# Kernel optimization log

Measured on AMD Instinct MI355X. Metric: run time of the kernel, lower is better.

## Reference

```python
import jax, jax.numpy as jnp
import numpy as np


def _dht(x):
    # Hartley transform via full fftn over ALL dims (matches torch dht2d(x, dim=None))
    f = jnp.fft.fftn(x)
    return f.real + f.imag


def setup_inputs() -> dict:
    key = jax.random.key(0)
    ks = jax.random.split(key, 5)
    B, H, W, C = 2, 128, 256, 768
    nb, fac = 8, 1
    bs = C // nb
    scale = 0.02
    x = jax.random.normal(ks[0], (B, H, W, C), dtype=jnp.float32)
    w1 = scale * jax.random.normal(ks[1], (2, nb, bs, bs * fac), dtype=jnp.float32)
    b1 = scale * jax.random.normal(ks[2], (2, nb, bs * fac), dtype=jnp.float32)
    w2 = scale * jax.random.normal(ks[3], (2, nb, bs * fac, bs), dtype=jnp.float32)
    b2 = scale * jax.random.normal(ks[4], (2, nb, bs), dtype=jnp.float32)
    return {"x": x, "w1": w1, "b1": b1, "w2": w2, "b2": b2}


def reference(x, w1, b1, w2, b2):
    SPARSITY = 0.01
    FRAC = 1.0  # hard_thresholding_fraction
    bias = x
    B, H, W, C = x.shape
    nb = w1.shape[1]
    bs = C // nb
    xf = x.astype(jnp.float32)

    X_k = _dht(xf).reshape(B, H, W, nb, bs)
    X_nk = jnp.roll(jnp.flip(xf, axis=(1, 2)), shift=(1, 1), axis=(1, 2)).reshape(B, H, W, nb, bs)

    total = H // 2 + 1
    kept = int(total * FRAC)
    r0, r1 = total - kept, min(total + kept, H)  # row slice clamps like torch slicing

    a = X_k[:, r0:r1, :kept]    # [B, Hs, kept, nb, bs]
    an = X_nk[:, r0:r1, :kept]

    ein = lambda t, w: jnp.einsum('bhwni,nio->bhwno', t, w)

    o1_k = jax.nn.relu(0.5 * (ein(a, w1[0]) - ein(an, w1[1]) + ein(a, w1[1]) + ein(an, w1[0])) + b1[0])
    o1_nk = jax.nn.relu(0.5 * (ein(an, w1[0]) - ein(a, w1[1]) + ein(an, w1[1]) + ein(a, w1[0])) + b1[1])

    o2_k = 0.5 * (ein(o1_k, w2[0]) - ein(o1_nk, w2[1]) + ein(o1_k, w2[1]) + ein(o1_nk, w2[0])) + b2[0]
    # NOTE: source genuinely uses o2_k (not o1_k) in two terms here; kept faithful.
    o2_nk = 0.5 * (ein(o1_nk, w2[0]) - ein(o2_k, w2[1]) + ein(o1_nk, w2[1]) + ein(o2_k, w2[0])) + b2[1]

    s = o2_k + o2_nk
    # softshrink
    s = jnp.sign(s) * jnp.maximum(jnp.abs(s) - SPARSITY, 0.0)

    full = jnp.zeros((B, H, W, nb, bs), jnp.float32).at[:, r0:r1, :kept].set(s)
    full = full.reshape(B, H, W, C)
    out = _dht(full) / full.size  # idht2d with dim=None: normalize by numel
    return out.astype(x.dtype) + bias
```

## Files before the change

kernel.cpp:

```cpp
#include <hip/hip_runtime.h>

#define BB 2
#define HH 128
#define WW 256
#define CC 768
#define NB 8
#define BS 96
#define WKEPT 65
#define NPTS (BB*HH*WKEPT)
#define NTOT ((size_t)BB*HH*WW*CC)
#define TWOPI 6.283185307179586f

#define P1_TW (9*127*8)
#define P7_TW (16*65*8)

__device__ __forceinline__ unsigned short f2bf(float f) {
    unsigned int u = __float_as_uint(f);
    u += 0x7fffu + ((u >> 16) & 1u);
    return (unsigned short)(u >> 16);
}
__device__ __forceinline__ float bf2f(unsigned short s) {
    return __uint_as_float((unsigned int)s << 16);
}

__global__ __launch_bounds__(256) void k_weights(
    const float* __restrict__ w2, const float* __restrict__ b2,
    float* __restrict__ WKP, float* __restrict__ WKM, float* __restrict__ BEFF)
{
    const int n = blockIdx.x;
    const int tid = threadIdx.x;
    __shared__ float m_s[BS*BS];

    const float* w2a = w2 + (size_t)(0*NB + n)*BS*BS;
    const float* w2b = w2 + (size_t)(1*NB + n)*BS*BS;
    for (int idx = tid; idx < BS*BS; idx += 256)
        m_s[idx] = 0.5f*(w2a[idx] - w2b[idx]);
    __syncthreads();

    for (int idx = tid; idx < BS*BS; idx += 256) {
        int i = idx / BS, o = idx - i*BS;
        float p_io = 0.5f*(w2a[idx] + w2b[idx]);
        float m_io = m_s[idx];
        float accK = 0.f, accN = 0.f;
        for (int j = 0; j < BS; ++j) {
            float p_ij = 0.5f*(w2a[i*BS + j] + w2b[i*BS + j]);
            float mjo  = m_s[j*BS + o];
            accK += p_ij * mjo;
            accN += m_s[i*BS + j] * mjo;
        }
        float valK = p_io + accK;
        float valN = p_io + m_io + accN;
        WKP[n*BS*BS + idx] = 0.5f*(valK + valN);
        WKM[n*BS*BS + idx] = 0.5f*(valK - valN);
    }
    if (tid < BS) {
        const float* b2a = b2 + (0*NB + n)*BS;
        const float* b2b = b2 + (1*NB + n)*BS;
        float acc = b2a[tid] + b2b[tid];
        for (int j = 0; j < BS; ++j) acc += b2a[j] * m_s[j*BS + tid];
        BEFF[n*BS + tid] = acc;
    }
}

__global__ __launch_bounds__(256) void k_tw(
    float* __restrict__ c7t, float* __restrict__ s7t)
{
    int idx = blockIdx.x*256 + threadIdx.x;
    if (idx < P7_TW) {
        int j = idx & 7; int rest = idx >> 3;
        int wq = rest % 65; int wg = rest / 65;
        int ai = ((wg*8 + j) * wq) & 255;
        float sn, cs; sincosf(TWOPI * (float)ai / 256.0f, &sn, &cs);
        c7t[idx] = cs; s7t[idx] = sn;
    }
}

__global__ __launch_bounds__(256) void k_p1(
    const float* __restrict__ x, float2* __restrict__ out)
{
    const int tid = threadIdx.x;
    const int row = blockIdx.y;
    const int c0 = blockIdx.x * 16;
    __shared__ float2 tw[256];
    __shared__ float2 bufA[8*256];
    __shared__ float2 bufB[8*256];

    {
        float sn, cs; sincosf(TWOPI*(float)tid/256.f, &sn, &cs);
        tw[tid] = make_float2(cs, -sn);
    }
    const float* xr = x + (size_t)row * WW * CC + c0;
    for (int idx = tid; idx < 2048; idx += 256) {
        int l = idx & 7, w = idx >> 3;
        const float2 v = *(const float2*)(xr + (size_t)w*CC + 2*l);
        bufA[l*256 + w] = v;
    }
    __syncthreads();

    float2* src = bufA;
    float2* dst = bufB;
    const int t  = tid & 127;
    const int l0 = tid >> 7;
    #pragma unroll
    for (int st = 0; st < 8; ++st) {
        const int s = 1 << st;
        const int q = t & (s - 1);
        const int p = t >> st;
        const float2 w = tw[p << st];
        #pragma unroll
        for (int k = 0; k < 4; ++k) {
            int base = (l0 + 2*k) * 256;
            float2 a = src[base + q + s*p];
            float2 b = src[base + q + s*p + 128];
            float dx = a.x - b.x, dy = a.y - b.y;
            dst[base + q + 2*s*p]     = make_float2(a.x + b.x, a.y + b.y);
            dst[base + q + 2*s*p + s] = make_float2(dx*w.x - dy*w.y, dx*w.y + dy*w.x);
        }
        __syncthreads();
        float2* tmp = src; src = dst; dst = tmp;
    }
    for (int idx = tid; idx < 8*WKEPT; idx += 256) {
        int l = idx & 7, wp = idx >> 3;
        float2 Z  = src[l*256 + wp];
        float2 Zm = src[l*256 + ((256 - wp) & 255)];
        float2 U = make_float2(0.5f*(Z.x + Zm.x), 0.5f*(Z.y - Zm.y));
        float2 V = make_float2(0.5f*(Z.y + Zm.y), 0.5f*(Zm.x - Z.x));
        size_t g = (size_t)(row*WKEPT + wp)*CC + c0 + 2*l;
        out[g]     = U;
        out[g + 1] = V;
    }
}

#define LPB 4
__global__ __launch_bounds__(256) void k_cfft(
    const float2* __restrict__ in, float2* __restrict__ out)
{
    __shared__ float2 tw[CC];
    __shared__ float2 bufA[LPB*CC];
    __shared__ float2 bufB[LPB*CC];
    const int tid = threadIdx.x;
    const size_t line0 = (size_t)blockIdx.x * LPB;

    for (int t = tid; t < CC; t += 256) {
        float sn, cs; sincosf(TWOPI * (float)t / 768.0f, &sn, &cs);
        tw[t] = make_float2(cs, -sn);
    }
    for (int idx = tid; idx < LPB*CC; idx += 256) {
        int l = idx / CC, c = idx - l*CC;
        int m = c / 3, j = c - 3*m;
        bufA[l*CC + j*256 + m] = in[(line0 + l)*CC + c];
    }
    __syncthreads();

    float2* src = bufA;
    float2* dst = bufB;
    #pragma unroll
    for (int st = 0; st < 8; ++st) {
        const int s = 1 << st;
        const int h = 128 >> st;
        for (int item = tid; item < LPB*3*128; item += 256) {
            int sub = item >> 7;
            int t   = item & 127;
            int q = t & (s - 1);
            int p = t >> st;
            float2 a = src[sub*256 + q + s*p];
            float2 b = src[sub*256 + q + s*(p + h)];
            float2 w = tw[p * (3 << st)];
            float dx = a.x - b.x, dy = a.y - b.y;
            dst[sub*256 + q + s*(2*p)]     = make_float2(a.x + b.x, a.y + b.y);
            dst[sub*256 + q + s*(2*p + 1)] = make_float2(dx*w.x - dy*w.y, dx*w.y + dy*w.x);
        }
        __syncthreads();
        float2* tmp = src; src = dst; dst = tmp;
    }
    for (int idx = tid; idx < LPB*CC; idx += 256) {
        int l = idx / CC, cp = idx - l*CC;
        int r = cp & 255;
        float2 S0 = src[(l*3 + 0)*256 + r];
        float2 S1 = src[(l*3 + 1)*256 + r];
        float2 S2 = src[(l*3 + 2)*256 + r];
        float2 w1 = tw[cp];
        int i2 = 2*cp; if (i2 >= CC) i2 -= CC;
        float2 w2 = tw[i2];
        float fr = S0.x + w1.x*S1.x - w1.y*S1.y + w2.x*S2.x - w2.y*S2.y;
        float fi = S0.y + w1.x*S1.y + w1.y*S1.x + w2.x*S2.y + w2.y*S2.x;
        out[(line0 + l)*CC + cp] = make_float2(fr, fi);
    }
}

__global__ __launch_bounds__(256) void k_hb_c2a(
    const float2* __restrict__ in, float* __restrict__ aout)
{
    const int tid = threadIdx.x;
    const int wp = blockIdx.y;
    const int c0 = blockIdx.x * 8;
    __shared__ float2 tw[128];
    __shared__ float2 bufA[16*128];
    __shared__ float2 bufB[16*128];

    if (tid < 128) {
        float sn, cs; sincosf(TWOPI*(float)tid/128.f, &sn, &cs);
        tw[tid] = make_float2(cs, -sn);
    }
    for (int idx = tid; idx < 1024; idx += 256) {
        int cl = idx & 7, h = idx >> 3;
        float2 z0 = in[(size_t)((0*HH + h)*WKEPT + wp)*CC + c0 + cl];
        float2 z1 = in[(size_t)((1*HH + h)*WKEPT + wp)*CC + c0 + cl];
        bufA[(2*cl+0)*128 + h] = make_float2(z0.x+z1.x, z0.y+z1.y);
        bufA[(2*cl+1)*128 + h] = make_float2(z0.x-z1.x, z0.y-z1.y);
    }
    __syncthreads();

    float2* src = bufA;
    float2* dst = bufB;
    const int t  = tid & 63;
    const int l0 = tid >> 6;
    #pragma unroll
    for (int st = 0; st < 7; ++st) {
        const int s = 1 << st;
        const int q = t & (s - 1);
        const int p = t >> st;
        const float2 w = tw[p << st];
        #pragma unroll
        for (int k = 0; k < 4; ++k) {
            int base = (l0 + 4*k) * 128;
            float2 a = src[base + q + s*p];
            float2 b = src[base + q + s*p + 64];
            float dx = a.x - b.x, dy = a.y - b.y;
            dst[base + q + 2*s*p]     = make_float2(a.x + b.x, a.y + b.y);
            dst[base + q + 2*s*p + s] = make_float2(dx*w.x - dy*w.y, dx*w.y + dy*w.x);
        }
        __syncthreads();
        float2* tmp = src; src = dst; dst = tmp;
    }
    for (int idx = tid; idx < 2048; idx += 256) {
        int cl = idx & 7;
        int hp = (idx >> 3) & 127;
        int uv = idx >> 10;
        float2 z = src[(2*cl + uv)*128 + hp];
        aout[(size_t)((uv*HH + hp)*WKEPT + wp)*CC + c0 + cl] = z.x + z.y;
    }
}

__global__ __launch_bounds__(256) void k_hb_s2c(
    const float* __restrict__ sreal, float2* __restrict__ out)
{
    const int tid = threadIdx.x;
    const int wp = blockIdx.y;
    const int c0 = blockIdx.x * 16;
    __shared__ float2 tw[128];
    __shared__ float2 bufA[16*128];
    __shared__ float2 bufB[16*128];

    if (tid < 128) {
        float sn, cs; sincosf(TWOPI*(float)tid/128.f, &sn, &cs);
        tw[tid] = make_float2(cs, -sn);
    }
    for (int idx = tid; idx < 2048; idx += 256) {
        int cl = idx & 15, h = idx >> 4;
        float s0 = sreal[(size_t)((0*HH + h)*WKEPT + wp)*CC + c0 + cl];
        float s1 = sreal[(size_t)((1*HH + h)*WKEPT + wp)*CC + c0 + cl];
        bufA[cl*128 + h] = make_float2(s0 + s1, s0 - s1);
    }
    __syncthreads();

    float2* src = bufA;
    float2* dst = bufB;
    const int t  = tid & 63;
    const int l0 = tid >> 6;
    #pragma unroll
    for (int st = 0; st < 7; ++st) {
        const int s = 1 << st;
        const int q = t & (s - 1);
        const int p = t >> st;
        const float2 w = tw[p << st];
        #pragma unroll
        for (int k = 0; k < 4; ++k) {
            int base = (l0 + 4*k) * 128;
            float2 a = src[base + q + s*p];
            float2 b = src[base + q + s*p + 64];
            float dx = a.x - b.x, dy = a.y - b.y;
            dst[base + q + 2*s*p]     = make_float2(a.x + b.x, a.y + b.y);
            dst[base + q + 2*s*p + s] = make_float2(dx*w.x - dy*w.y, dx*w.y + dy*w.x);
        }
        __syncthreads();
        float2* tmp = src; src = dst; dst = tmp;
    }
    for (int idx = tid; idx < 2048; idx += 256) {
        int cl = idx & 15;
        int hp = idx >> 4;
        float2 A  = src[cl*128 + hp];
        float2 Zm = src[cl*128 + ((128 - hp) & 127)];
        float2 U = make_float2(0.5f*(A.x + Zm.x), 0.5f*(A.y - Zm.y));
        float2 V = make_float2(0.5f*(A.y + Zm.y), 0.5f*(Zm.x - A.x));
        out[(size_t)((0*HH + hp)*WKEPT + wp)*CC + c0 + cl] = U;
        out[(size_t)((1*HH + hp)*WKEPT + wp)*CC + c0 + cl] = V;
    }
}

__global__ __launch_bounds__(256, 6) void k_mlp(
    const float* __restrict__ a, const float* __restrict__ x,
    const float* __restrict__ w1, const float* __restrict__ b1,
    const float* __restrict__ WKP, const float* __restrict__ WKM,
    const float* __restrict__ BEFF, float* __restrict__ sout)
{
    const int tid = threadIdx.x;
    const int n = blockIdx.y;
    const int P0 = blockIdx.x * 64;
    __shared__ unsigned short SH[2*96*67];
    unsigned short* As = SH;
    unsigned short* Bs = SH + 96*67;

    for (int idx = tid; idx < 64*96; idx += 256) {
        int p = idx / 96, i = idx - p*96;
        int P = P0 + p;
        float av = a[(size_t)P*CC + n*BS + i];
        int b = P / (HH*WKEPT);
        int rem = P - b*(HH*WKEPT);
        int h = rem / WKEPT;
        int wq = rem - h*WKEPT;
        int hh2 = (HH - h) & (HH-1);
        int ww2 = (WW - wq) & (WW-1);
        float anv = x[(size_t)((b*HH + hh2)*WW + ww2)*CC + n*BS + i];
        As[i*67 + p] = f2bf(0.5f*(av + anv));
        Bs[i*67 + p] = f2bf(0.5f*(av - anv));
    }
    __syncthreads();

    const int lane = tid & 63;
    const int wv = __builtin_amdgcn_readfirstlane(tid >> 6);
    const int ob = wv * 24;

    float t1[24], t2[24];
    #pragma unroll
    for (int j = 0; j < 24; ++j) { t1[j] = 0.f; t2[j] = 0.f; }
    {
        const float* w10 = w1 + (size_t)(0*NB + n)*BS*BS + ob;
        const float* w11 = w1 + (size_t)(1*NB + n)*BS*BS + ob;
        #pragma unroll 2
        for (int i = 0; i < 96; ++i) {
            float Uv = bf2f(As[i*67 + lane]);
            float Vv = bf2f(Bs[i*67 + lane]);
            const float* r0 = w10 + i*BS;
            const float* r1 = w11 + i*BS;
            #pragma unroll
            for (int j = 0; j < 24; ++j) {
                t1[j] = fmaf(Uv, r0[j], t1[j]);
                t2[j] = fmaf(Vv, r1[j], t2[j]);
            }
        }
    }

    {
        const float* b1k = b1 + (0*NB + n)*BS + ob;
        const float* b1n = b1 + (1*NB + n)*BS + ob;
        float p2v[24], m2v[24];
        #pragma unroll
        for (int j = 0; j < 24; ++j) {
            float ok = fmaxf(t1[j] + t2[j] + b1k[j], 0.f);
            float on = fmaxf(t1[j] - t2[j] + b1n[j], 0.f);
            p2v[j] = ok + on;
            m2v[j] = ok - on;
        }
        __syncthreads();
        #pragma unroll
        for (int j = 0; j < 24; ++j) {
            As[(ob + j)*67 + lane] = f2bf(p2v[j]);
            Bs[(ob + j)*67 + lane] = f2bf(m2v[j]);
        }
        __syncthreads();
    }

    float acc[24];
    #pragma unroll
    for (int j = 0; j < 24; ++j) acc[j] = 0.f;
    {
        const float* wkp = WKP + n*BS*BS + ob;
        const float* wkm = WKM + n*BS*BS + ob;
        #pragma unroll 2
        for (int i = 0; i < 96; ++i) {
            float pv = bf2f(As[i*67 + lane]);
            float mv = bf2f(Bs[i*67 + lane]);
            const float* rk = wkp + i*BS;
            const float* rm = wkm + i*BS;
            #pragma unroll
            for (int j = 0; j < 24; ++j) {
                acc[j] = fmaf(pv, rk[j], fmaf(mv, rm[j], acc[j]));
            }
        }
    }

    {
        const float* be = BEFF + n*BS + ob;
        float r[24];
        #pragma unroll
        for (int j = 0; j < 24; ++j) {
            float v = acc[j] + be[j];
            float av2 = fabsf(v) - 0.01f;
            r[j] = (av2 > 0.f) ? copysignf(av2, v) : 0.f;
        }
        __syncthreads();
        float* Fs = (float*)SH;
        #pragma unroll
        for (int j = 0; j < 24; ++j)
            Fs[lane*97 + ob + j] = r[j];
        __syncthreads();
        for (int idx = tid; idx < 64*96; idx += 256) {
            int p2i = idx / 96, o = idx - p2i*96;
            sout[(size_t)(P0 + p2i)*CC + n*BS + o] = Fs[p2i*97 + o];
        }
    }
}

__global__ __launch_bounds__(256) void k_p7(
    const float2* __restrict__ A, const float* __restrict__ x,
    const float* __restrict__ c7t, const float* __restrict__ s7t,
    float* __restrict__ out)
{
    const int tid = threadIdx.x;
    const int ct = blockIdx.x % 3;
    const int wg = blockIdx.x / 3;
    const int rg = blockIdx.y;
    const int c  = ct*256 + tid;
    const int wpb = wg*8;
    const int row0 = rg*4;

    float accA[4][8], accB[4][8], acc128[4];
    #pragma unroll
    for (int r = 0; r < 4; ++r) {
        acc128[r] = 0.f;
        #pragma unroll
        for (int j = 0; j < 8; ++j) { accA[r][j] = 0.f; accB[r][j] = 0.f; }
    }

    const float2* A0 = A + (size_t)row0 * WKEPT * CC + c;
    const float4* cT = (const float4*)(c7t + (size_t)wg*65*8);
    const float4* sT = (const float4*)(s7t + (size_t)wg*65*8);
    for (int wq = 0; wq < 65; ++wq) {
        float4 c0 = cT[2*wq], c1 = cT[2*wq+1];
        float4 s0 = sT[2*wq], s1 = sT[2*wq+1];
        float sg = (wq & 1) ? -1.f : 1.f;
        #pragma unroll
        for (int r = 0; r < 4; ++r) {
            float2 v = A0[(size_t)(r*WKEPT + wq) * CC];
            float P = v.x + v.y;
            float M = v.y - v.x;
            float N = v.x - v.y;
            acc128[r] = fmaf(sg, P, acc128[r]);
            accA[r][0] = fmaf(P, c0.x, fmaf(M, s0.x, accA[r][0]));
            accB[r][0] = fmaf(P, c0.x, fmaf(N, s0.x, accB[r][0]));
            accA[r][1] = fmaf(P, c0.y, fmaf(M, s0.y, accA[r][1]));
            accB[r][1] = fmaf(P, c0.y, fmaf(N, s0.y, accB[r][1]));
            accA[r][2] = fmaf(P, c0.z, fmaf(M, s0.z, accA[r][2]));
            accB[r][2] = fmaf(P, c0.z, fmaf(N, s0.z, accB[r][2]));
            accA[r][3] = fmaf(P, c0.w, fmaf(M, s0.w, accA[r][3]));
            accB[r][3] = fmaf(P, c0.w, fmaf(N, s0.w, accB[r][3]));
            accA[r][4] = fmaf(P, c1.x, fmaf(M, s1.x, accA[r][4]));
            accB[r][4] = fmaf(P, c1.x, fmaf(N, s1.x, accB[r][4]));
            accA[r][5] = fmaf(P, c1.y, fmaf(M, s1.y, accA[r][5]));
            accB[r][5] = fmaf(P, c1.y, fmaf(N, s1.y, accB[r][5]));
            accA[r][6] = fmaf(P, c1.z, fmaf(M, s1.z, accA[r][6]));
            accB[r][6] = fmaf(P, c1.z, fmaf(N, s1.z, accB[r][6]));
            accA[r][7] = fmaf(P, c1.w, fmaf(M, s1.w, accA[r][7]));
            accB[r][7] = fmaf(P, c1.w, fmaf(N, s1.w, accB[r][7]));
        }
    }

    const float scale = 1.0f / 50331648.0f;
    #pragma unroll
    for (int r = 0; r < 4; ++r) {
        size_t base = (size_t)(row0 + r) * WW * CC + c;
        #pragma unroll
        for (int j = 0; j < 8; ++j) {
            int w = wpb + j;
            size_t g = base + (size_t)w*CC;
            out[g] = fmaf(accA[r][j], scale, x[g]);
            if (w != 0) {
                size_t g2 = base + (size_t)(256 - w)*CC;
                out[g2] = fmaf(accB[r][j], scale, x[g2]);
            }
        }
        if (wg == 0) {
            size_t g = base + (size_t)128*CC;
            out[g] = fmaf(acc128[r], scale, x[g]);
        }
    }
}

__global__ __launch_bounds__(256) void k_p7_fb(
    const float2* __restrict__ A, const float* __restrict__ x,
    float* __restrict__ out)
{
    const int tid = threadIdx.x;
    const int ct = blockIdx.x % 3;
    const int wg = blockIdx.x / 3;
    const int h = blockIdx.y, b = blockIdx.z;
    const int c = ct*256 + tid;
    __shared__ float cm[WKEPT][8];
    __shared__ float cp[WKEPT][8];
    for (int idx = tid; idx < WKEPT*8; idx += 256) {
        int wq = idx >> 3, j = idx & 7;
        int w = wg*8 + j;
        int ai = (w * wq) & 255;
        float sn, cse; sincosf(TWOPI * (float)ai / 256.f, &sn, &cse);
        cm[wq][j] = cse - sn;
        cp[wq][j] = cse + sn;
    }
    __syncthreads();
    float acc[8] = {0,0,0,0,0,0,0,0};
    const float2* Ab = A + (size_t)((b*HH + h)*WKEPT)*CC + c;
    for (int wq = 0; wq < WKEPT; ++wq) {
        float2 v = Ab[(size_t)wq*CC];
        const float4* m4 = (const float4*)(&cm[wq][0]);
        const float4* p4 = (const float4*)(&cp[wq][0]);
        #pragma unroll
        for (int jj = 0; jj < 2; ++jj) {
            float4 qm = m4[jj], qp = p4[jj];
            acc[4*jj+0] += v.x*qm.x + v.y*qp.x;
            acc[4*jj+1] += v.x*qm.y + v.y*qp.y;
            acc[4*jj+2] += v.x*qm.z + v.y*qp.z;
            acc[4*jj+3] += v.x*qm.w + v.y*qp.w;
        }
    }
    const float scale = 1.0f / 50331648.0f;
    size_t base = (size_t)(b*HH + h)*WW*CC + c;
    #pragma unroll
    for (int j = 0; j < 8; ++j) {
        int w = wg*8 + j;
        size_t g = base + (size_t)w*CC;
        out[g] = fmaf(acc[j], scale, x[g]);
    }
}

extern "C" void kernel_launch(void* const* d_in, const int* in_sizes, int n_in,
                              void* d_out, int out_size, void* d_ws, size_t ws_size,
                              hipStream_t stream)
{
    (void)in_sizes; (void)n_in; (void)out_size;
    const float* x  = (const float*)d_in[0];
    const float* w1 = (const float*)d_in[1];
    const float* b1 = (const float*)d_in[2];
    const float* w2 = (const float*)d_in[3];
    const float* b2 = (const float*)d_in[4];

    float*  ws     = (float*)d_ws;
    float2* Abuf   = (float2*)d_ws;
    float*  a_real = ws;
    float*  s_real = ws + (size_t)NPTS*CC;
    float*  W1P    = ws + 2*(size_t)NPTS*CC;
    float*  W1M    = W1P + NB*BS*BS;
    float*  WKP    = W1M + NB*BS*BS;
    float*  WKM    = WKP + NB*BS*BS;
    float*  BEFF   = WKM + NB*BS*BS;
    float*  c1t    = BEFF + NB*BS;
    float*  s1t    = c1t + P1_TW;
    float*  c7t    = s1t + P1_TW;
    float*  s7t    = c7t + P7_TW;

    const size_t need_bytes =
        ((size_t)2*NPTS*CC + 4*(size_t)NB*BS*BS + NB*BS + 2*P1_TW + 2*P7_TW)
        * sizeof(float);
    const bool fast = (ws_size >= need_bytes);

    float2* Bc   = (float2*)d_out;
    float*  outf = (float*)d_out;

    k_weights<<<dim3(NB), dim3(256), 0, stream>>>(w2, b2, WKP, WKM, BEFF);
    if (fast) {
        k_tw<<<dim3(33), dim3(256), 0, stream>>>(c7t, s7t);
    }
    k_p1     <<<dim3(48, 256), dim3(256), 0, stream>>>(x, Abuf);
    k_cfft   <<<dim3(NPTS/LPB), dim3(256), 0, stream>>>(Abuf, Bc);
    k_hb_c2a <<<dim3(96, WKEPT), dim3(256), 0, stream>>>(Bc, a_real);
    k_mlp    <<<dim3(260, NB), dim3(256), 0, stream>>>(a_real, x, w1, b1,
                                                       WKP, WKM, BEFF, s_real);
    k_hb_s2c <<<dim3(48, WKEPT), dim3(256), 0, stream>>>(s_real, Bc);
    k_cfft   <<<dim3(NPTS/LPB), dim3(256), 0, stream>>>(Bc, Abuf);
    if (fast) {
        k_p7<<<dim3(48, 64), dim3(256), 0, stream>>>(Abuf, x, c7t, s7t, outf);
    } else {
        k_p7_fb<<<dim3(96, HH, BB), dim3(256), 0, stream>>>(Abuf, x, outf);
    }
}
```

Measured before the change: 1.187 ms.

## Move block-diagonal MLP to bf16 MFMA with hi/lo split weights

Rewrites the per-block MLP kernel to use 16x16x32 bf16 MFMA instructions instead of scalar FP32 FMAs. Weights are pre-split in the prep kernel into high and low bf16 parts, transposed, and staged through shared memory in K-chunks, which keeps weight precision close to FP32 while activations stay bf16. This targets the FMA-bound GEMM inside the MLP stage. The cost is twice the MFMA work for the hi/lo split, extra workspace for the split weights, and a lower occupancy hint.

```diff
diff --git a/kernel.cpp b/kernel.cpp
--- a/kernel.cpp
+++ b/kernel.cpp
@@ -11,8 +11,10 @@
 #define NTOT ((size_t)BB*HH*WW*CC)
 #define TWOPI 6.283185307179586f
 
-#define P1_TW (9*127*8)
 #define P7_TW (16*65*8)
+
+typedef __attribute__((ext_vector_type(8))) short bf16x8;
+typedef __attribute__((ext_vector_type(4))) float f32x4;
 
 __device__ __forceinline__ unsigned short f2bf(float f) {
     unsigned int u = __float_as_uint(f);
@@ -24,8 +26,13 @@
 }
 
 __global__ __launch_bounds__(256) void k_weights(
-    const float* __restrict__ w2, const float* __restrict__ b2,
-    float* __restrict__ WKP, float* __restrict__ WKM, float* __restrict__ BEFF)
+    const float* __restrict__ w1, const float* __restrict__ w2,
+    const float* __restrict__ b2,
+    unsigned short* __restrict__ W10h, unsigned short* __restrict__ W10l,
+    unsigned short* __restrict__ W11h, unsigned short* __restrict__ W11l,
+    unsigned short* __restrict__ WKPh, unsigned short* __restrict__ WKPl,
+    unsigned short* __restrict__ WKMh, unsigned short* __restrict__ WKMl,
+    float* __restrict__ BEFF)
 {
     const int n = blockIdx.x;
     const int tid = threadIdx.x;
@@ -35,6 +42,20 @@
     const float* w2b = w2 + (size_t)(1*NB + n)*BS*BS;
     for (int idx = tid; idx < BS*BS; idx += 256)
         m_s[idx] = 0.5f*(w2a[idx] - w2b[idx]);
+
+    const float* w1a = w1 + (size_t)(0*NB + n)*BS*BS;
+    const float* w1b = w1 + (size_t)(1*NB + n)*BS*BS;
+    for (int idx = tid; idx < BS*BS; idx += 256) {
+        int o = idx / BS, k = idx - o*BS;
+        float v0 = w1a[k*BS + o];
+        unsigned short h0 = f2bf(v0);
+        unsigned short l0 = f2bf(v0 - bf2f(h0));
+        W10h[n*BS*BS + idx] = h0;  W10l[n*BS*BS + idx] = l0;
+        float v1 = w1b[k*BS + o];
+        unsigned short h1 = f2bf(v1);
+        unsigned short l1 = f2bf(v1 - bf2f(h1));
+        W11h[n*BS*BS + idx] = h1;  W11l[n*BS*BS + idx] = l1;
+    }
     __syncthreads();
 
     for (int idx = tid; idx < BS*BS; idx += 256) {
@@ -50,8 +71,13 @@
         }
         float valK = p_io + accK;
         float valN = p_io + m_io + accN;
-        WKP[n*BS*BS + idx] = 0.5f*(valK + valN);
-        WKM[n*BS*BS + idx] = 0.5f*(valK - valN);
+        float wkp = 0.5f*(valK + valN);
+        float wkm = 0.5f*(valK - valN);
+        int d = n*BS*BS + o*BS + i;
+        unsigned short hp = f2bf(wkp);
+        WKPh[d] = hp;  WKPl[d] = f2bf(wkp - bf2f(hp));
+        unsigned short hm = f2bf(wkm);
+        WKMh[d] = hm;  WKMl[d] = f2bf(wkm - bf2f(hm));
     }
     if (tid < BS) {
         const float* b2a = b2 + (0*NB + n)*BS;
@@ -298,116 +324,141 @@
     }
 }
 
-__global__ __launch_bounds__(256, 6) void k_mlp(
+__global__ __launch_bounds__(256, 2) void k_mlp(
     const float* __restrict__ a, const float* __restrict__ x,
-    const float* __restrict__ w1, const float* __restrict__ b1,
-    const float* __restrict__ WKP, const float* __restrict__ WKM,
-    const float* __restrict__ BEFF, float* __restrict__ sout)
+    const unsigned short* __restrict__ W10h, const unsigned short* __restrict__ W10l,
+    const unsigned short* __restrict__ W11h, const unsigned short* __restrict__ W11l,
+    const unsigned short* __restrict__ WKPh, const unsigned short* __restrict__ WKPl,
+    const unsigned short* __restrict__ WKMh, const unsigned short* __restrict__ WKMl,
+    const float* __restrict__ b1, const float* __restrict__ BEFF,
+    float* __restrict__ sout)
 {
     const int tid = threadIdx.x;
     const int n = blockIdx.y;
     const int P0 = blockIdx.x * 64;
-    __shared__ unsigned short SH[2*96*67];
-    unsigned short* As = SH;
-    unsigned short* Bs = SH + 96*67;
-
-    for (int idx = tid; idx < 64*96; idx += 256) {
-        int p = idx / 96, i = idx - p*96;
-        int P = P0 + p;
-        float av = a[(size_t)P*CC + n*BS + i];
-        int b = P / (HH*WKEPT);
-        int rem = P - b*(HH*WKEPT);
-        int h = rem / WKEPT;
-        int wq = rem - h*WKEPT;
-        int hh2 = (HH - h) & (HH-1);
-        int ww2 = (WW - wq) & (WW-1);
-        float anv = x[(size_t)((b*HH + hh2)*WW + ww2)*CC + n*BS + i];
-        As[i*67 + p] = f2bf(0.5f*(av + anv));
-        Bs[i*67 + p] = f2bf(0.5f*(av - anv));
-    }
-    __syncthreads();
+    __shared__ unsigned short Wh_A[96*48], Wl_A[96*48];
+    __shared__ unsigned short Wh_B[96*48], Wl_B[96*48];
+    __shared__ unsigned short PMp[64*104], PMm[64*104];
 
     const int lane = tid & 63;
-    const int wv = __builtin_amdgcn_readfirstlane(tid >> 6);
-    const int ob = wv * 24;
-
-    float t1[24], t2[24];
-    #pragma unroll
-    for (int j = 0; j < 24; ++j) { t1[j] = 0.f; t2[j] = 0.f; }
-    {
-        const float* w10 = w1 + (size_t)(0*NB + n)*BS*BS + ob;
-        const float* w11 = w1 + (size_t)(1*NB + n)*BS*BS + ob;
-        #pragma unroll 2
-        for (int i = 0; i < 96; ++i) {
-            float Uv = bf2f(As[i*67 + lane]);
-            float Vv = bf2f(Bs[i*67 + lane]);
-            const float* r0 = w10 + i*BS;
-            const float* r1 = w11 + i*BS;
-            #pragma unroll
-            for (int j = 0; j < 24; ++j) {
-                t1[j] = fmaf(Uv, r0[j], t1[j]);
-                t2[j] = fmaf(Vv, r1[j], t2[j]);
-            }
-        }
-    }
-
-    {
-        const float* b1k = b1 + (0*NB + n)*BS + ob;
-        const float* b1n = b1 + (1*NB + n)*BS + ob;
-        float p2v[24], m2v[24];
-        #pragma unroll
-        for (int j = 0; j < 24; ++j) {
-            float ok = fmaxf(t1[j] + t2[j] + b1k[j], 0.f);
-            float on = fmaxf(t1[j] - t2[j] + b1n[j], 0.f);
-            p2v[j] = ok + on;
-            m2v[j] = ok - on;
-        }
-        __syncthreads();
-        #pragma unroll
-        for (int j = 0; j < 24; ++j) {
-            As[(ob + j)*67 + lane] = f2bf(p2v[j]);
-            Bs[(ob + j)*67 + lane] = f2bf(m2v[j]);
-        }
-        __syncthreads();
-    }
-
-    float acc[24];
-    #pragma unroll
-    for (int j = 0; j < 24; ++j) acc[j] = 0.f;
-    {
-        const float* wkp = WKP + n*BS*BS + ob;
-        const float* wkm = WKM + n*BS*BS + ob;
-        #pragma unroll 2
-        for (int i = 0; i < 96; ++i) {
-            float pv = bf2f(As[i*67 + lane]);
-            float mv = bf2f(Bs[i*67 + lane]);
-            const float* rk = wkp + i*BS;
-            const float* rm = wkm + i*BS;
-            #pragma unroll
-            for (int j = 0; j < 24; ++j) {
-                acc[j] = fmaf(pv, rk[j], fmaf(mv, rm[j], acc[j]));
-            }
-        }
-    }
-
-    {
-        const float* be = BEFF + n*BS + ob;
-        float r[24];
-        #pragma unroll
-        for (int j = 0; j < 24; ++j) {
-            float v = acc[j] + be[j];
+    const int wv = tid >> 6;
+    const int lr = lane & 15;
+    const int lk = lane >> 4;
+
+    const int Pld = P0 + 16*wv + lr;
+    int bb = Pld / (HH*WKEPT);
+    int rem = Pld - bb*(HH*WKEPT);
+    int h = rem / WKEPT;
+    int wq = rem - h*WKEPT;
+    int hh2 = (HH - h) & (HH-1);
+    int ww2 = (WW - wq) & (WW-1);
+    const float* aRow  = a + (size_t)Pld*CC + n*BS;
+    const float* anRow = x + (size_t)((bb*HH + hh2)*WW + ww2)*CC + n*BS;
+
+    f32x4 T1[6], T2[6];
+    #pragma unroll
+    for (int t = 0; t < 6; ++t) {
+        T1[t] = (f32x4){0.f,0.f,0.f,0.f};
+        T2[t] = (f32x4){0.f,0.f,0.f,0.f};
+    }
+
+    for (int ks = 0; ks < 3; ++ks) {
+        __syncthreads();
+        for (int idx = tid; idx < 96*16; idx += 256) {
+            int o = idx >> 4, kp = (idx & 15) << 1;
+            int g = n*BS*BS + o*BS + ks*32 + kp;
+            *(ushort2*)&Wh_A[o*48 + kp] = *(const ushort2*)&W10h[g];
+            *(ushort2*)&Wl_A[o*48 + kp] = *(const ushort2*)&W10l[g];
+            *(ushort2*)&Wh_B[o*48 + kp] = *(const ushort2*)&W11h[g];
+            *(ushort2*)&Wl_B[o*48 + kp] = *(const ushort2*)&W11l[g];
+        }
+        __syncthreads();
+
+        const int kseg = ks*32 + 8*lk;
+        float4 a0 = *(const float4*)(aRow + kseg);
+        float4 a1 = *(const float4*)(aRow + kseg + 4);
+        float4 n0 = *(const float4*)(anRow + kseg);
+        float4 n1 = *(const float4*)(anRow + kseg + 4);
+        bf16x8 uF, vF;
+        uF[0] = (short)f2bf(0.5f*(a0.x + n0.x));  vF[0] = (short)f2bf(0.5f*(a0.x - n0.x));
+        uF[1] = (short)f2bf(0.5f*(a0.y + n0.y));  vF[1] = (short)f2bf(0.5f*(a0.y - n0.y));
+        uF[2] = (short)f2bf(0.5f*(a0.z + n0.z));  vF[2] = (short)f2bf(0.5f*(a0.z - n0.z));
+        uF[3] = (short)f2bf(0.5f*(a0.w + n0.w));  vF[3] = (short)f2bf(0.5f*(a0.w - n0.w));
+        uF[4] = (short)f2bf(0.5f*(a1.x + n1.x));  vF[4] = (short)f2bf(0.5f*(a1.x - n1.x));
+        uF[5] = (short)f2bf(0.5f*(a1.y + n1.y));  vF[5] = (short)f2bf(0.5f*(a1.y - n1.y));
+        uF[6] = (short)f2bf(0.5f*(a1.z + n1.z));  vF[6] = (short)f2bf(0.5f*(a1.z - n1.z));
+        uF[7] = (short)f2bf(0.5f*(a1.w + n1.w));  vF[7] = (short)f2bf(0.5f*(a1.w - n1.w));
+
+        #pragma unroll
+        for (int t = 0; t < 6; ++t) {
+            int wb = (16*t + lr)*48 + 8*lk;
+            bf16x8 bh = *(const bf16x8*)&Wh_A[wb];
+            T1[t] = __builtin_amdgcn_mfma_f32_16x16x32_bf16(uF, bh, T1[t], 0, 0, 0);
+            bf16x8 bl = *(const bf16x8*)&Wl_A[wb];
+            T1[t] = __builtin_amdgcn_mfma_f32_16x16x32_bf16(uF, bl, T1[t], 0, 0, 0);
+            bf16x8 ch = *(const bf16x8*)&Wh_B[wb];
+            T2[t] = __builtin_amdgcn_mfma_f32_16x16x32_bf16(vF, ch, T2[t], 0, 0, 0);
+            bf16x8 cl = *(const bf16x8*)&Wl_B[wb];
+            T2[t] = __builtin_amdgcn_mfma_f32_16x16x32_bf16(vF, cl, T2[t], 0, 0, 0);
+        }
+    }
+
+    #pragma unroll
+    for (int t = 0; t < 6; ++t) {
+        float bk = b1[(0*NB + n)*BS + 16*t + lr];
+        float bn = b1[(1*NB + n)*BS + 16*t + lr];
+        #pragma unroll
+        for (int r = 0; r < 4; ++r) {
+            float ok = fmaxf(T1[t][r] + T2[t][r] + bk, 0.f);
+            float on = fmaxf(T1[t][r] - T2[t][r] + bn, 0.f);
+            int pl = 16*wv + 4*lk + r;
+            PMp[pl*104 + 16*t + lr] = f2bf(ok + on);
+            PMm[pl*104 + 16*t + lr] = f2bf(ok - on);
+        }
+    }
+
+    f32x4 S[6];
+    #pragma unroll
+    for (int t = 0; t < 6; ++t) S[t] = (f32x4){0.f,0.f,0.f,0.f};
+    for (int ks = 0; ks < 3; ++ks) {
+        __syncthreads();
+        for (int idx = tid; idx < 96*16; idx += 256) {
+            int o = idx >> 4, kp = (idx & 15) << 1;
+            int g = n*BS*BS + o*BS + ks*32 + kp;
+            *(ushort2*)&Wh_A[o*48 + kp] = *(const ushort2*)&WKPh[g];
+            *(ushort2*)&Wl_A[o*48 + kp] = *(const ushort2*)&WKPl[g];
+            *(ushort2*)&Wh_B[o*48 + kp] = *(const ushort2*)&WKMh[g];
+            *(ushort2*)&Wl_B[o*48 + kp] = *(const ushort2*)&WKMl[g];
+        }
+        __syncthreads();
+
+        const int kseg = ks*32 + 8*lk;
+        bf16x8 pF = *(const bf16x8*)&PMp[(16*wv + lr)*104 + kseg];
+        bf16x8 mF = *(const bf16x8*)&PMm[(16*wv + lr)*104 + kseg];
+        #pragma unroll
+        for (int t = 0; t < 6; ++t) {
+            int wb = (16*t + lr)*48 + 8*lk;
+            bf16x8 bh = *(const bf16x8*)&Wh_A[wb];
+            S[t] = __builtin_amdgcn_mfma_f32_16x16x32_bf16(pF, bh, S[t], 0, 0, 0);
+            bf16x8 bl = *(const bf16x8*)&Wl_A[wb];
+            S[t] = __builtin_amdgcn_mfma_f32_16x16x32_bf16(pF, bl, S[t], 0, 0, 0);
+            bf16x8 ch = *(const bf16x8*)&Wh_B[wb];
+            S[t] = __builtin_amdgcn_mfma_f32_16x16x32_bf16(mF, ch, S[t], 0, 0, 0);
+            bf16x8 cl = *(const bf16x8*)&Wl_B[wb];
+            S[t] = __builtin_amdgcn_mfma_f32_16x16x32_bf16(mF, cl, S[t], 0, 0, 0);
+        }
+    }
+
+    #pragma unroll
+    for (int t = 0; t < 6; ++t) {
+        float be = BEFF[n*BS + 16*t + lr];
+        #pragma unroll
+        for (int r = 0; r < 4; ++r) {
+            float v = S[t][r] + be;
             float av2 = fabsf(v) - 0.01f;
-            r[j] = (av2 > 0.f) ? copysignf(av2, v) : 0.f;
-        }
-        __syncthreads();
-        float* Fs = (float*)SH;
-        #pragma unroll
-        for (int j = 0; j < 24; ++j)
-            Fs[lane*97 + ob + j] = r[j];
-        __syncthreads();
-        for (int idx = tid; idx < 64*96; idx += 256) {
-            int p2i = idx / 96, o = idx - p2i*96;
-            sout[(size_t)(P0 + p2i)*CC + n*BS + o] = Fs[p2i*97 + o];
+            float sv = (av2 > 0.f) ? copysignf(av2, v) : 0.f;
+            int pt = P0 + 16*wv + 4*lk + r;
+            sout[(size_t)pt*CC + n*BS + 16*t + lr] = sv;
         }
     }
 }
@@ -547,33 +598,38 @@
     float2* Abuf   = (float2*)d_ws;
     float*  a_real = ws;
     float*  s_real = ws + (size_t)NPTS*CC;
-    float*  W1P    = ws + 2*(size_t)NPTS*CC;
-    float*  W1M    = W1P + NB*BS*BS;
-    float*  WKP    = W1M + NB*BS*BS;
-    float*  WKM    = WKP + NB*BS*BS;
-    float*  BEFF   = WKM + NB*BS*BS;
-    float*  c1t    = BEFF + NB*BS;
-    float*  s1t    = c1t + P1_TW;
-    float*  c7t    = s1t + P1_TW;
+    float*  BEFF   = ws + 2*(size_t)NPTS*CC;
+    float*  c7t    = BEFF + NB*BS;
     float*  s7t    = c7t + P7_TW;
+    unsigned short* Wq = (unsigned short*)(s7t + P7_TW);
+    const size_t WSZ = (size_t)NB*BS*BS;
+    unsigned short* W10h = Wq + 0*WSZ;
+    unsigned short* W10l = Wq + 1*WSZ;
+    unsigned short* W11h = Wq + 2*WSZ;
+    unsigned short* W11l = Wq + 3*WSZ;
+    unsigned short* WKPh = Wq + 4*WSZ;
+    unsigned short* WKPl = Wq + 5*WSZ;
+    unsigned short* WKMh = Wq + 6*WSZ;
+    unsigned short* WKMl = Wq + 7*WSZ;
 
     const size_t need_bytes =
-        ((size_t)2*NPTS*CC + 4*(size_t)NB*BS*BS + NB*BS + 2*P1_TW + 2*P7_TW)
-        * sizeof(float);
+        ((size_t)2*NPTS*CC + NB*BS + 2*P7_TW)*4 + 8*WSZ*2;
     const bool fast = (ws_size >= need_bytes);
 
     float2* Bc   = (float2*)d_out;
     float*  outf = (float*)d_out;
 
-    k_weights<<<dim3(NB), dim3(256), 0, stream>>>(w2, b2, WKP, WKM, BEFF);
+    k_weights<<<dim3(NB), dim3(256), 0, stream>>>(
+        w1, w2, b2, W10h, W10l, W11h, W11l, WKPh, WKPl, WKMh, WKMl, BEFF);
     if (fast) {
         k_tw<<<dim3(33), dim3(256), 0, stream>>>(c7t, s7t);
     }
     k_p1     <<<dim3(48, 256), dim3(256), 0, stream>>>(x, Abuf);
     k_cfft   <<<dim3(NPTS/LPB), dim3(256), 0, stream>>>(Abuf, Bc);
     k_hb_c2a <<<dim3(96, WKEPT), dim3(256), 0, stream>>>(Bc, a_real);
-    k_mlp    <<<dim3(260, NB), dim3(256), 0, stream>>>(a_real, x, w1, b1,
-                                                       WKP, WKM, BEFF, s_real);
+    k_mlp    <<<dim3(260, NB), dim3(256), 0, stream>>>(
+        a_real, x, W10h, W10l, W11h, W11l, WKPh, WKPl, WKMh, WKMl,
+        b1, BEFF, s_real);
     k_hb_s2c <<<dim3(48, WKEPT), dim3(256), 0, stream>>>(s_real, Bc);
     k_cfft   <<<dim3(NPTS/LPB), dim3(256), 0, stream>>>(Bc, Abuf);
     if (fast) {
```

New measurement: 1.086 ms. 1.09x faster.
